# Kernel tuning notes

Hardware: AMD Instinct MI355X
Metric: run time of the kernel (lower is better)

The kernel has to match this reference:

```python
import jax, jax.numpy as jnp
import numpy as np

B, T, BIN, D, S, L = 128, 512, 24, 256, 128, 2
MAX_LEN = 512.0   # config.max_length, used as attention score scale
EPS = 1e-6
P = 3.0           # GeM pooling power


def _sinusoid(t, dim, min_ts=1.0, max_ts=10000.0):
    # half sin / half cos geometric timescales (min_timescale..max_timescale)
    num = dim // 2
    inv = min_ts * jnp.exp(jnp.arange(num, dtype=jnp.float32) * (-np.log(max_ts / min_ts) / max(num - 1, 1)))
    ang = jnp.arange(t, dtype=jnp.float32)[:, None] * inv[None, :]        # [T, dim/2]
    return jnp.concatenate([jnp.sin(ang), jnp.cos(ang)], axis=-1)          # [T, dim]


def _rope(x):
    # rotate-half RoPE over last dim, positions along axis -2
    t, d = x.shape[-2], x.shape[-1]
    inv = 1.0 / (10000.0 ** (jnp.arange(0, d, 2, dtype=jnp.float32) / d))  # [d/2]
    ang = jnp.arange(t, dtype=jnp.float32)[:, None] * inv[None, :]         # [T, d/2]
    sin = jnp.concatenate([jnp.sin(ang), jnp.sin(ang)], axis=-1)
    cos = jnp.concatenate([jnp.cos(ang), jnp.cos(ang)], axis=-1)
    x1, x2 = jnp.split(x, 2, axis=-1)
    return x * cos + jnp.concatenate([-x2, x1], axis=-1) * sin


def setup_inputs() -> dict:
    key = jax.random.key(0)
    ks = jax.random.split(key, 12)
    std_in = 1.0 / np.sqrt(BIN)
    std_d = 1.0 / np.sqrt(D)
    return {
        "x": jax.random.uniform(ks[0], (B, T, BIN), dtype=jnp.float32),
        "pe_scale": jnp.ones((), jnp.float32),                                  # learnable PE scale
        "W_in": jax.random.normal(ks[1], (BIN, D), jnp.float32) * std_in,        # encoder_start
        "b_in": jnp.zeros((D,), jnp.float32),
        "norm_scale": jnp.ones((L,), jnp.float32),                               # ScaledNorm scalar per layer
        "W1": jax.random.normal(ks[2], (L, D, 2 * D + S), jnp.float32) * std_d,  # GAU in-proj
        "b1": jnp.zeros((L, 2 * D + S), jnp.float32),
        "gamma": jnp.ones((L, 2, S), jnp.float32),                               # q/k offset-scale
        "beta": jnp.zeros((L, 2, S), jnp.float32),
        "W2": jax.random.normal(ks[3], (L, D, D), jnp.float32) * std_d,          # GAU out-proj
        "b2": jnp.zeros((L, D), jnp.float32),
        "We": jax.random.normal(ks[4], (D, D), jnp.float32) * std_d,             # metric embedding
        "be": jnp.zeros((D,), jnp.float32),
    }


def reference(x, pe_scale, W_in, b_in, norm_scale, W1, b1, gamma, beta, W2, b2, We, be):
    # scaled sinusoidal positional embedding (additive)
    h = x + pe_scale * _sinusoid(x.shape[1], x.shape[2])
    # encoder start + swish
    h = jax.nn.swish(h @ W_in + b_in)                                   # [B,T,D]
    for i in range(L):  # GAU stack (attention-free gated attention units)
        shortcut = h
        hn = h * jax.lax.rsqrt(jnp.mean(h * h, axis=-1, keepdims=True) + EPS) * norm_scale[i]
        uv = jax.nn.swish(hn @ W1[i] + b1[i])                           # [B,T,2D+S]
        u, v, base = uv[..., :D], uv[..., D:2 * D], uv[..., 2 * D:]
        q = _rope(base * gamma[i, 0] + beta[i, 0])                      # [B,T,S]
        k = _rope(base * gamma[i, 1] + beta[i, 1])
        scores = jnp.einsum('bnd,bmd->bnm', q, k) / MAX_LEN             # [B,T,T]
        attn = jnp.square(jax.nn.relu(scores))                          # SqrReLU
        out = u * jnp.einsum('bnm,bme->bne', attn, v)                   # gated attention output
        h = shortcut + out @ W2[i] + b2[i]
    unpooled = h
    # generalized-mean pooling over sequence (p=3, clamp for stability)
    pooled = jnp.mean(jnp.clip(h, EPS, None) ** P, axis=1) ** (1.0 / P)  # [B,D]
    # metric embedding: linear + L2 normalize
    emb = pooled @ We + be
    emb = emb / jnp.linalg.norm(emb, axis=-1, keepdims=True)
    return emb, unpooled
```

## Files before the change

kernel.cpp:

```cpp
#include <hip/hip_runtime.h>
#include <hip/hip_bf16.h>

#define B_ 128
#define T_ 512
#define BIN_ 24
#define D_ 256
#define S_ 128
#define L_ 2
#define BT_ (B_*T_)

typedef __hip_bfloat16 bf16;
typedef __hip_bfloat162 bf162;
typedef __attribute__((ext_vector_type(8))) short bf16x8;
typedef __attribute__((ext_vector_type(4))) short s16x4;
typedef __attribute__((ext_vector_type(4))) float f32x4;

__device__ __forceinline__ float b2f(bf16 x){ return __bfloat162float(x); }
__device__ __forceinline__ bf16 f2b(float x){ return __float2bfloat16(x); }
__device__ __forceinline__ float swish(float v){
  float e = __builtin_amdgcn_exp2f(-1.442695040888963f * v);
  return v * __builtin_amdgcn_rcpf(1.f + e);
}
__device__ __forceinline__ void gld16(const bf16* g, bf16* l){
  __builtin_amdgcn_global_load_lds(
      (const __attribute__((address_space(1))) void*)g,
      (__attribute__((address_space(3))) void*)l, 16, 0, 0);
}

__global__ void tables_kernel(const float* pe_scale_ptr, float* pe_tab, float* rs, float* rc) {
  int t = blockIdx.x;
  int j = threadIdx.x;
  float ps = pe_scale_ptr[0];
  const float LOG1E4 = 9.210340371976184f;
  if (j < 64) {
    float inv = expf(-LOG1E4 * (float)j / 64.f);
    float ang = (float)t * inv;
    rs[t*64 + j] = sinf(ang);
    rc[t*64 + j] = cosf(ang);
  }
  if (j < BIN_) {
    int jj = (j < 12) ? j : (j - 12);
    float inv = expf(-LOG1E4 * (float)jj / 11.f);
    float ang = (float)t * inv;
    pe_tab[t*BIN_ + j] = ps * ((j < 12) ? sinf(ang) : cosf(ang));
  }
}

__global__ __launch_bounds__(256) void prep_kernel(const float* W1, const float* W2,
                                                   bf16* W1t, bf16* W2t) {
  int idx = blockIdx.x*256 + threadIdx.x;
  if (idx < 2*256*640) {
    int l = idx / (256*640); int rem = idx % (256*640);
    int k = rem / 640; int n = rem % 640;
    W1t[(size_t)l*640*256 + n*256 + k] = f2b(W1[idx]);
  }
  if (idx < 2*256*256) {
    int l = idx >> 16; int rem = idx & 65535;
    int k = rem >> 8; int n = rem & 255;
    W2t[(size_t)l*65536 + n*256 + k] = f2b(W2[idx]);
  }
}

__global__ __launch_bounds__(256) void init_kernel(float* rms1, float* pooled_raw) {
  int i = blockIdx.x*256 + threadIdx.x;
  if (i < BT_) rms1[i] = 0.f;
  if (i < B_*D_) pooled_raw[i] = 0.f;
}

__global__ __launch_bounds__(256) void embed_kernel(const float* x, const float* pe_tab,
                const float* W_in, const float* b_in, float* h, float* rms0, bf16* hb) {
  __shared__ float xr[8][BIN_];
  __shared__ float wsum[4][8];
  int tid = threadIdx.x;
  int row0 = blockIdx.x * 8;
  if (tid < 8*BIN_) {
    int r = tid / BIN_, k = tid % BIN_;
    int row = row0 + r;
    int t = row & (T_-1);
    xr[r][k] = x[(size_t)row*BIN_ + k] + pe_tab[t*BIN_ + k];
  }
  __syncthreads();
  int d = tid;
  float bi = b_in[d];
  float acc[8];
  #pragma unroll
  for (int r=0;r<8;r++) acc[r]=bi;
  #pragma unroll
  for (int k=0;k<BIN_;k++){
    float w = W_in[k*D_ + d];
    #pragma unroll
    for (int r=0;r<8;r++) acc[r] += xr[r][k]*w;
  }
  float sq[8];
  #pragma unroll
  for (int r=0;r<8;r++){
    float v = swish(acc[r]);
    h[(size_t)(row0+r)*D_ + d] = v;
    hb[(size_t)(row0+r)*D_ + d] = f2b(v);
    sq[r] = v*v;
  }
  #pragma unroll
  for (int off=1; off<64; off<<=1)
    #pragma unroll
    for (int r=0;r<8;r++) sq[r] += __shfl_xor(sq[r], off);
  if ((tid&63)==0)
    #pragma unroll
    for (int r=0;r<8;r++) wsum[tid>>6][r] = sq[r];
  __syncthreads();
  if (tid < 8) rms0[row0+tid] = wsum[0][tid]+wsum[1][tid]+wsum[2][tid]+wsum[3][tid];
}

__global__ __launch_bounds__(256) void gemm1_mfma(const bf16* A, const bf16* Bt,
      const float* bias, const float* rmsraw, const float* norm_scale, int l,
      bf16* u, bf16* Vtg, bf16* basebuf) {
  __shared__ char smem[34816];
  bf16* As  = (bf16*)smem;
  bf16* Bs  = (bf16*)(smem + 16384);
  bf16* Ovl = (bf16*)smem;

  int tid = threadIdx.x;
  int w = tid>>6, lane = tid&63, r = lane&15, g = lane>>4;
  int wr = w>>1, wc = w&1;
  int dd = blockIdx.x; int xcd = dd&7, slot = dd>>3;
  int panel = xcd*64 + slot/5; int bx = slot%5;
  int row0 = panel*128, col0 = bx*128;

  int trl = 8*w + (lane>>3);
  int tcg = ((lane&7) ^ ((lane>>3)&7)) * 8;

  f32x4 acc[4][4];
  #pragma unroll
  for (int i=0;i<4;i++)
    #pragma unroll
    for (int j=0;j<4;j++) acc[i][j] = (f32x4){0.f,0.f,0.f,0.f};

  for (int k0=0; k0<D_; k0+=64) {
    #pragma unroll
    for (int i=0;i<4;i++){
      int tr = 32*i + trl;
      gld16(A  + (size_t)(row0+tr)*D_ + k0 + tcg, As + (32*i + 8*w)*64);
      gld16(Bt + (size_t)(col0+tr)*D_ + k0 + tcg, Bs + (32*i + 8*w)*64);
    }
    __syncthreads();
    #pragma unroll
    for (int kk=0; kk<2; kk++){
      bf16x8 a[4], b[4];
      #pragma unroll
      for (int i=0;i<4;i++){
        int ch = ((kk*4 + g) ^ (r&7)) * 8;
        a[i] = *(const bf16x8*)(As + (64*wr+16*i+r)*64 + ch);
        b[i] = *(const bf16x8*)(Bs + (64*wc+16*i+r)*64 + ch);
      }
      #pragma unroll
      for (int i=0;i<4;i++)
        #pragma unroll
        for (int j=0;j<4;j++)
          acc[i][j] = __builtin_amdgcn_mfma_f32_16x16x32_bf16(a[i], b[j], acc[i][j], 0,0,0);
    }
    __syncthreads();
  }

  float ns = norm_scale[l];
  #pragma unroll
  for (int i=0;i<4;i++){
    size_t grow0 = row0 + 64*wr + 16*i + 4*g;
    float4 rv = *(const float4*)(rmsraw + grow0);
    float sc[4];
    sc[0] = rsqrtf(rv.x*(1.f/D_) + 1e-6f) * ns;
    sc[1] = rsqrtf(rv.y*(1.f/D_) + 1e-6f) * ns;
    sc[2] = rsqrtf(rv.z*(1.f/D_) + 1e-6f) * ns;
    sc[3] = rsqrtf(rv.w*(1.f/D_) + 1e-6f) * ns;
    #pragma unroll
    for (int j=0;j<4;j++){
      int gcol = col0 + 64*wc + 16*j + r;
      float bv = bias[gcol];
      if (bx < 2) {
        #pragma unroll
        for (int reg=0; reg<4; reg++){
          float v = swish(acc[i][j][reg]*sc[reg] + bv);
          u[(grow0+reg)*D_ + gcol] = f2b(v);
        }
      } else if (bx < 4) {
        #pragma unroll
        for (int reg=0; reg<4; reg++){
          float v = swish(acc[i][j][reg]*sc[reg] + bv);
          Ovl[(64*wc+16*j+r)*136 + (64*wr+16*i+4*g+reg)] = f2b(v);
        }
      } else {
        #pragma unroll
        for (int reg=0; reg<4; reg++){
          float v = swish(acc[i][j][reg]*sc[reg] + bv);
          basebuf[(grow0+reg)*S_ + (gcol-512)] = f2b(v);
        }
      }
    }
  }

  if (bx == 2 || bx == 3) {
    __syncthreads();
    size_t bb = row0 >> 9;
    int mg = row0 & 511;
    #pragma unroll
    for (int c=0;c<8;c++){
      int chunk = c*256 + tid;
      int e = chunk >> 4, mloc = (chunk & 15)*8;
      *(bf16x8*)(Vtg + bb*131072 + (size_t)(col0-256+e)*T_ + mg + mloc) =
        *(const bf16x8*)(Ovl + e*136 + mloc);
    }
  }
}

__global__ __launch_bounds__(256) void qk_kernel(const bf16* basebuf, const float* gamma, const float* beta,
      int l, const float* rs, const float* rc, bf16* q, bf16* k) {
  int tid = threadIdx.x;
  int j = tid & 127;
  size_t row = (size_t)blockIdx.x*2 + (tid>>7);
  int t = (int)(row & (T_-1));
  int j2 = j ^ 64;
  float v0 = b2f(basebuf[row*S_ + j]);
  float v1 = b2f(basebuf[row*S_ + j2]);
  int jm = j & 63;
  float sn = rs[t*64 + jm], cs = rc[t*64 + jm];
  float sgn = (j < 64) ? -1.f : 1.f;
  const float* g  = gamma + l*2*S_;
  const float* bt = beta  + l*2*S_;
  float xq = v0*g[j]      + bt[j];
  float pq = v1*g[j2]     + bt[j2];
  q[row*S_ + j] = f2b(xq*cs + sgn*pq*sn);
  float xk = v0*g[S_+j]   + bt[S_+j];
  float pk = v1*g[S_+j2]  + bt[S_+j2];
  k[row*S_ + j] = f2b(xk*cs + sgn*pk*sn);
}

__global__ __launch_bounds__(512, 4) void attn_gemm2_fused(const bf16* q, const bf16* k,
      const bf16* Vtg, const bf16* u, const bf16* W2t, const float* bias,
      float* h, int mode, float* rms1, float* pooled_raw, float* outb, bf16* hb) {
  __shared__ char smem[77824];
  bf16* Ks = (bf16*)smem;
  bf16* Vt = (bf16*)(smem + 17408);
  bf16* Ps = (bf16*)(smem + 50176);
  bf16* Os = (bf16*)smem;
  bf16* Wt = (bf16*)(smem + 67584);

  int tid = threadIdx.x;
  int w = tid >> 6, l = tid & 63;
  int r = l & 15, g = l >> 4;
  int xcd = blockIdx.x & 7, j0 = blockIdx.x >> 3;
  int b  = xcd*16 + (j0 >> 2);
  int nt = j0 & 3;
  size_t rowbase = (size_t)b * T_;
  int n0 = nt * 128;

  bf16x8 qf[4];
  const bf16* qrow = q + (rowbase + n0 + 16*w + r) * S_ + g*8;
  #pragma unroll
  for (int kk=0; kk<4; kk++) qf[kk] = *(const bf16x8*)(qrow + kk*32);

  f32x4 oacc[16];
  #pragma unroll
  for (int i=0;i<16;i++) oacc[i] = (f32x4){0.f,0.f,0.f,0.f};

  for (int m0 = 0; m0 < T_; m0 += 64) {
    #pragma unroll
    for (int i=0;i<2;i++){
      int chunk = i*512 + tid;
      int row = chunk >> 4, c = chunk & 15;
      *(bf16x8*)(Ks + row*136 + c*8) =
        *(const bf16x8*)(k + (rowbase + m0 + row)*S_ + c*8);
    }
    #pragma unroll
    for (int i=0;i<4;i++){
      int chunk = i*512 + tid;
      int e = chunk >> 3, c = chunk & 7;
      *(bf16x8*)(Vt + e*64 + ((c ^ (e&7)) << 3)) =
        *(const bf16x8*)(Vtg + (size_t)b*131072 + (size_t)e*T_ + m0 + c*8);
    }
    __syncthreads();

    #pragma unroll
    for (int nf=0; nf<4; nf++){
      f32x4 sacc = (f32x4){0.f,0.f,0.f,0.f};
      #pragma unroll
      for (int kk=0; kk<4; kk++){
        bf16x8 kf = *(const bf16x8*)(Ks + (16*nf + r)*136 + kk*32 + g*8);
        sacc = __builtin_amdgcn_mfma_f32_16x16x32_bf16(qf[kk], kf, sacc, 0,0,0);
      }
      #pragma unroll
      for (int reg=0; reg<4; reg++){
        float t = fmaxf(sacc[reg] * (1.f/512.f), 0.f);
        Ps[(16*w + 4*g + reg)*72 + 16*nf + r] = f2b(t*t);
      }
    }
    #pragma unroll
    for (int ks=0; ks<2; ks++){
      bf16x8 pa = *(const bf16x8*)(Ps + (16*w + r)*72 + ks*32 + g*8);
      #pragma unroll
      for (int nf2=0; nf2<16; nf2++){
        int e = 16*nf2 + r;
        bf16x8 vb = *(const bf16x8*)(Vt + e*64 + (((4*ks + g) ^ (e&7)) << 3));
        oacc[nf2] = __builtin_amdgcn_mfma_f32_16x16x32_bf16(pa, vb, oacc[nf2], 0,0,0);
      }
    }
    __syncthreads();
  }

  size_t growbase = rowbase + n0;
  #pragma unroll
  for (int nf2=0; nf2<16; nf2++){
    #pragma unroll
    for (int reg=0; reg<4; reg++){
      Os[(16*w + 4*g + reg)*264 + 16*nf2 + r] = f2b(oacc[nf2][reg]);
    }
  }
  __syncthreads();
  #pragma unroll
  for (int i=0;i<8;i++){
    int chunk = i*512 + tid;
    int row = chunk >> 5, c = chunk & 31;
    bf16x8 uvv = *(const bf16x8*)(u + (growbase + row)*D_ + c*8);
    bf16x8 ov  = *(const bf16x8*)(Os + row*264 + c*8);
    bf16x8 res;
    #pragma unroll
    for (int e=0;e<8;e++)
      ((bf16*)&res)[e] = f2b(b2f(((bf16*)&ov)[e]) * b2f(((bf16*)&uvv)[e]));
    *(bf16x8*)(Os + row*264 + c*8) = res;
  }
  #pragma unroll
  for (int i=0;i<16;i++) oacc[i] = (f32x4){0.f,0.f,0.f,0.f};
  __syncthreads();

  for (int kc=0; kc<8; kc++){
    bf16x8 a0 = *(const bf16x8*)(Os + (16*w + r)*264 + kc*32 + g*8);
    #pragma unroll
    for (int nh=0; nh<2; nh++){
      __syncthreads();
      {
        int rowW = tid>>2, ko = (tid&3)*8;
        *(bf16x8*)(Wt + rowW*40 + ko) =
          *(const bf16x8*)(W2t + (size_t)(128*nh + rowW)*256 + kc*32 + ko);
      }
      __syncthreads();
      #pragma unroll
      for (int nf2h=0; nf2h<8; nf2h++){
        bf16x8 bfr = *(const bf16x8*)(Wt + (16*nf2h + r)*40 + g*8);
        oacc[nh*8+nf2h] =
          __builtin_amdgcn_mfma_f32_16x16x32_bf16(a0, bfr, oacc[nh*8+nf2h], 0,0,0);
      }
    }
  }

  if (mode == 0) {
    #pragma unroll
    for (int reg=0; reg<4; reg++){
      size_t row = growbase + 16*w + 4*g + reg;
      float ssum = 0.f;
      #pragma unroll
      for (int nf2=0; nf2<16; nf2++){
        int col = 16*nf2 + r;
        float hv = h[row*D_ + col] + oacc[nf2][reg] + bias[col];
        h[row*D_ + col] = hv;
        hb[row*D_ + col] = f2b(hv);
        ssum += hv*hv;
      }
      ssum += __shfl_xor(ssum,1); ssum += __shfl_xor(ssum,2);
      ssum += __shfl_xor(ssum,4); ssum += __shfl_xor(ssum,8);
      if (r == 0) rms1[row] = ssum;
    }
  } else {
    #pragma unroll
    for (int nf2=0; nf2<16; nf2++){
      int col = 16*nf2 + r;
      float bv = bias[col];
      float psum = 0.f;
      #pragma unroll
      for (int reg=0; reg<4; reg++){
        size_t row = growbase + 16*w + 4*g + reg;
        float hv = h[row*D_ + col] + oacc[nf2][reg] + bv;
        outb[row*D_ + col] = hv;
        float cv = fmaxf(hv, 1e-6f);
        psum += cv*cv*cv;
      }
      psum += __shfl_xor(psum,16); psum += __shfl_xor(psum,32);
      if (g == 0) atomicAdd(pooled_raw + b*D_ + col, psum);
    }
  }
}

__global__ __launch_bounds__(256) void emb_kernel(const float* pooled_raw, const float* We,
      const float* be, float* out) {
  __shared__ float pr[D_];
  __shared__ float red[256];
  int b = blockIdx.x, j = threadIdx.x;
  pr[j] = cbrtf(pooled_raw[b*D_+j] * (1.f/T_));
  __syncthreads();
  float acc = be[j];
  for (int kk=0;kk<D_;kk++) acc += pr[kk]*We[kk*D_+j];
  red[j] = acc*acc;
  __syncthreads();
  for (int off=128; off>0; off>>=1){
    if (j<off) red[j]+=red[j+off];
    __syncthreads();
  }
  out[b*D_+j] = acc * rsqrtf(red[0]);
}

extern "C" void kernel_launch(void* const* d_in, const int* in_sizes, int n_in,
                              void* d_out, int out_size, void* d_ws, size_t ws_size,
                              hipStream_t stream) {
  const float* x         = (const float*)d_in[0];
  const float* pe_scale  = (const float*)d_in[1];
  const float* W_in      = (const float*)d_in[2];
  const float* b_in      = (const float*)d_in[3];
  const float* norm_scale= (const float*)d_in[4];
  const float* W1        = (const float*)d_in[5];
  const float* b1        = (const float*)d_in[6];
  const float* gamma     = (const float*)d_in[7];
  const float* beta      = (const float*)d_in[8];
  const float* W2        = (const float*)d_in[9];
  const float* b2        = (const float*)d_in[10];
  const float* We        = (const float*)d_in[11];
  const float* be        = (const float*)d_in[12];

  char* ws = (char*)d_ws;
  float* h       = (float*)(ws);
  bf16*  hb      = (bf16*)(ws + 67108864);
  bf16*  u       = (bf16*)(ws + 100663296);
  bf16*  Vtg     = (bf16*)(ws + 134217728);
  bf16*  basebuf = (bf16*)(ws + 167772160);
  bf16*  q       = (bf16*)(ws + 184549376);
  bf16*  kbuf    = (bf16*)(ws + 201326592);
  float* pe_tab  = (float*)(ws + 218103808);
  float* rs_tab  = (float*)(ws + 218152960);
  float* rc_tab  = (float*)(ws + 218284032);
  float* pooled_raw = (float*)(ws + 218415104);
  float* rms0    = (float*)(ws + 218546176);
  float* rms1    = (float*)(ws + 218808320);
  bf16*  W1t     = (bf16*)(ws + 219070464);
  bf16*  W2t     = (bf16*)(ws + 219725824);

  tables_kernel<<<T_, 64, 0, stream>>>(pe_scale, pe_tab, rs_tab, rc_tab);
  prep_kernel<<<1280, 256, 0, stream>>>(W1, W2, W1t, W2t);
  init_kernel<<<BT_/256, 256, 0, stream>>>(rms1, pooled_raw);
  embed_kernel<<<BT_/8, 256, 0, stream>>>(x, pe_tab, W_in, b_in, h, rms0, hb);
  float* outb = (float*)d_out + B_*D_;
  for (int l=0; l<L_; l++) {
    gemm1_mfma<<<BT_/128*5, 256, 0, stream>>>(hb, W1t + (size_t)l*640*D_, b1 + l*640,
        l ? rms1 : rms0, norm_scale, l, u, Vtg, basebuf);
    qk_kernel<<<BT_/2, 256, 0, stream>>>(basebuf, gamma, beta, l, rs_tab, rc_tab, q, kbuf);
    attn_gemm2_fused<<<B_*4, 512, 0, stream>>>(q, kbuf, Vtg, u,
        W2t + (size_t)l*D_*D_, b2 + l*D_, h, l, rms1, pooled_raw, outb, hb);
  }
  emb_kernel<<<B_, 256, 0, stream>>>(pooled_raw, We, be, (float*)d_out);
}
```

Baseline: 371.7 us.

## Switch attention QK and PV matmuls to 32x32x16 MFMA with 2D wave tiling

```diff
diff --git a/kernel.cpp b/kernel.cpp
--- a/kernel.cpp
+++ b/kernel.cpp
@@ -14,6 +14,7 @@
 typedef __attribute__((ext_vector_type(8))) short bf16x8;
 typedef __attribute__((ext_vector_type(4))) short s16x4;
 typedef __attribute__((ext_vector_type(4))) float f32x4;
+typedef __attribute__((ext_vector_type(16))) float f32x16;
 
 __device__ __forceinline__ float b2f(bf16 x){ return __bfloat162float(x); }
 __device__ __forceinline__ bf16 f2b(float x){ return __float2bfloat16(x); }
@@ -245,20 +246,22 @@
   int tid = threadIdx.x;
   int w = tid >> 6, l = tid & 63;
   int r = l & 15, g = l >> 4;
+  int l31 = l & 31, l5 = l >> 5;
+  int rg = w & 3, cg = w >> 2;
   int xcd = blockIdx.x & 7, j0 = blockIdx.x >> 3;
   int b  = xcd*16 + (j0 >> 2);
   int nt = j0 & 3;
   size_t rowbase = (size_t)b * T_;
   int n0 = nt * 128;
 
-  bf16x8 qf[4];
-  const bf16* qrow = q + (rowbase + n0 + 16*w + r) * S_ + g*8;
-  #pragma unroll
-  for (int kk=0; kk<4; kk++) qf[kk] = *(const bf16x8*)(qrow + kk*32);
-
-  f32x4 oacc[16];
-  #pragma unroll
-  for (int i=0;i<16;i++) oacc[i] = (f32x4){0.f,0.f,0.f,0.f};
+  bf16x8 qf[8];
+  const bf16* qrow = q + (rowbase + n0 + 32*rg + l31) * S_ + l5*8;
+  #pragma unroll
+  for (int kk=0; kk<8; kk++) qf[kk] = *(const bf16x8*)(qrow + kk*16);
+
+  f32x16 oacc4[4];
+  #pragma unroll
+  for (int i=0;i<4;i++) oacc4[i] = (f32x16)(0.f);
 
   for (int m0 = 0; m0 < T_; m0 += 64) {
     #pragma unroll
@@ -277,28 +280,29 @@
     }
     __syncthreads();
 
-    #pragma unroll
-    for (int nf=0; nf<4; nf++){
-      f32x4 sacc = (f32x4){0.f,0.f,0.f,0.f};
-      #pragma unroll
-      for (int kk=0; kk<4; kk++){
-        bf16x8 kf = *(const bf16x8*)(Ks + (16*nf + r)*136 + kk*32 + g*8);
-        sacc = __builtin_amdgcn_mfma_f32_16x16x32_bf16(qf[kk], kf, sacc, 0,0,0);
-      }
-      #pragma unroll
-      for (int reg=0; reg<4; reg++){
-        float t = fmaxf(sacc[reg] * (1.f/512.f), 0.f);
-        Ps[(16*w + 4*g + reg)*72 + 16*nf + r] = f2b(t*t);
-      }
-    }
-    #pragma unroll
-    for (int ks=0; ks<2; ks++){
-      bf16x8 pa = *(const bf16x8*)(Ps + (16*w + r)*72 + ks*32 + g*8);
-      #pragma unroll
-      for (int nf2=0; nf2<16; nf2++){
-        int e = 16*nf2 + r;
-        bf16x8 vb = *(const bf16x8*)(Vt + e*64 + (((4*ks + g) ^ (e&7)) << 3));
-        oacc[nf2] = __builtin_amdgcn_mfma_f32_16x16x32_bf16(pa, vb, oacc[nf2], 0,0,0);
+    f32x16 sacc = (f32x16)(0.f);
+    #pragma unroll
+    for (int kk=0; kk<8; kk++){
+      bf16x8 kf = *(const bf16x8*)(Ks + (32*cg + l31)*136 + kk*16 + l5*8);
+      sacc = __builtin_amdgcn_mfma_f32_32x32x16_bf16(qf[kk], kf, sacc, 0,0,0);
+    }
+    #pragma unroll
+    for (int reg=0; reg<16; reg++){
+      float t = fmaxf(sacc[reg] * (1.f/512.f), 0.f);
+      int rloc = (reg&3) + 8*(reg>>2) + 4*l5;
+      Ps[(32*rg + rloc)*72 + 32*cg + l31] = f2b(t*t);
+    }
+    __syncthreads();
+
+    #pragma unroll
+    for (int ks4=0; ks4<4; ks4++){
+      bf16x8 pa = *(const bf16x8*)(Ps + (32*rg + l31)*72 + ks4*16 + l5*8);
+      #pragma unroll
+      for (int nt4=0; nt4<4; nt4++){
+        int e = 128*cg + 32*nt4 + l31;
+        int chunk = (ks4*2 + l5) ^ (e&7);
+        bf16x8 vb = *(const bf16x8*)(Vt + e*64 + (chunk << 3));
+        oacc4[nt4] = __builtin_amdgcn_mfma_f32_32x32x16_bf16(pa, vb, oacc4[nt4], 0,0,0);
       }
     }
     __syncthreads();
@@ -306,10 +310,11 @@
 
   size_t growbase = rowbase + n0;
   #pragma unroll
-  for (int nf2=0; nf2<16; nf2++){
-    #pragma unroll
-    for (int reg=0; reg<4; reg++){
-      Os[(16*w + 4*g + reg)*264 + 16*nf2 + r] = f2b(oacc[nf2][reg]);
+  for (int nt4=0; nt4<4; nt4++){
+    #pragma unroll
+    for (int reg=0; reg<16; reg++){
+      int rloc = (reg&3) + 8*(reg>>2) + 4*l5;
+      Os[(32*rg + rloc)*264 + 128*cg + 32*nt4 + l31] = f2b(oacc4[nt4][reg]);
     }
   }
   __syncthreads();
@@ -325,6 +330,7 @@
       ((bf16*)&res)[e] = f2b(b2f(((bf16*)&ov)[e]) * b2f(((bf16*)&uvv)[e]));
     *(bf16x8*)(Os + row*264 + c*8) = res;
   }
+  f32x4 oacc[16];
   #pragma unroll
   for (int i=0;i<16;i++) oacc[i] = (f32x4){0.f,0.f,0.f,0.f};
   __syncthreads();
```

Result: slower. 401.7 us (+8.1%).
